# Kernel tuning notes

Hardware: AMD Instinct MI355X
Metric: run time of the kernel (lower is better)

The kernel has to match this reference:

```python
import jax, jax.numpy as jnp
import numpy as np

D_MODEL = 1024
D_CONV = 3

def setup_inputs() -> dict:
    key = jax.random.key(0)
    ks = jax.random.split(key, 16)
    d = D_MODEL
    s = 1.0 / np.sqrt(d)
    inp = {
        'x': jax.random.normal(ks[0], (4, 4096, d), dtype=jnp.float32),
        'Wq_w': jax.random.normal(ks[1], (d, d), dtype=jnp.float32) * s,
        'Wq_b': jnp.zeros((d,), dtype=jnp.float32),
        'Wo_w': jax.random.normal(ks[2], (d, d), dtype=jnp.float32) * s,
        'Wo_b': jnp.zeros((d,), dtype=jnp.float32),
        'Wg_w': jax.random.normal(ks[3], (d, d), dtype=jnp.float32) * s,
        'Wg_b': jnp.zeros((d,), dtype=jnp.float32),
        'wa_w': jax.random.normal(ks[4], (d, d), dtype=jnp.float32) * s,
        'wb_w': jax.random.normal(ks[5], (d, d), dtype=jnp.float32) * s,
        'Wout_w': jax.random.normal(ks[6], (d, d), dtype=jnp.float32) * s,
        'Wout_b': jnp.zeros((d,), dtype=jnp.float32),
        'conv_w': jax.random.normal(ks[7], (d, d, D_CONV), dtype=jnp.float32) * (1.0 / np.sqrt(d * D_CONV)),
        'conv_b': jnp.zeros((d,), dtype=jnp.float32),
    }
    return inp

def _lin(x, w, b=None):
    y = jnp.einsum('bsd,ed->bse', x, w)
    return y if b is None else y + b

def _summ(x_to, x_from, w, scale):
    # gelu -> linear -> softmax over seq -> weighted sum over seq -> broadcast
    a = jax.nn.softmax(_lin(jax.nn.gelu(x_from, approximate=False), w) * scale, axis=-2)
    return jnp.sum(x_to * a, axis=-2, keepdims=True)  # [B,1,d], broadcasts

def reference(x, Wq_w, Wq_b, Wo_w, Wo_b, Wg_w, Wg_b, wa_w, wb_w, Wout_w, Wout_b, conv_w, conv_b):
    d = x.shape[-1]
    scale = 1.0 / jnp.sqrt(jnp.asarray(d, x.dtype))
    Q = _lin(x, Wq_w, Wq_b)
    O = _lin(x, Wo_w, Wo_b)
    G = _lin(x, Wg_w, Wg_b)
    # conv1d over sequence: [B,S,d] -> [B,d,S] -> conv -> back
    qt = jnp.transpose(Q, (0, 2, 1))
    ct = jax.lax.conv_general_dilated(qt, conv_w, window_strides=(1,),
                                      padding=[(D_CONV // 2, D_CONV // 2)],
                                      dimension_numbers=('NCH', 'OIH', 'NCH'))
    ct = ct + conv_b[None, :, None]
    cq = jax.nn.silu(jnp.transpose(ct, (0, 2, 1)))
    P = O * _summ(Q, cq, wa_w, scale)
    L = jax.nn.silu(G) * _summ(P, P, wb_w, scale)
    return _lin(L, Wout_w, Wout_b)
```

## Files before the change

### kernel.cpp

```cpp
#include <hip/hip_runtime.h>
#include <stdint.h>

#define DEV __device__ __forceinline__

typedef unsigned short u16;
typedef unsigned int u32;
typedef unsigned char u8;

typedef __bf16 bf16x8 __attribute__((ext_vector_type(8)));
typedef float f32x4 __attribute__((ext_vector_type(4)));
typedef u16 u16x8 __attribute__((ext_vector_type(8)));
typedef u16 u16x4 __attribute__((ext_vector_type(4)));
typedef u8 u8x8 __attribute__((ext_vector_type(8)));
typedef int i32x4 __attribute__((ext_vector_type(4)));
typedef int i32x8 __attribute__((ext_vector_type(8)));

static_assert(sizeof(bf16x8) == 16, "bf16x8 must be 16B");

#define NT 16384
#define SPAD 4098

DEV u16 f2bf(float f) {
  u32 u = __float_as_uint(f);
  u32 r = u + 0x7FFFu + ((u >> 16) & 1u);
  return (u16)(r >> 16);
}
DEV float bf2f(u16 h) { return __uint_as_float(((u32)h) << 16); }
DEV float siluf(float x) { return x / (1.f + __expf(-x)); }
DEV float geluf(float x) { return 0.5f * x * (1.f + erff(x * 0.70710678118654752f)); }

DEV u8 f2fp8(float f) {
  u32 u = __float_as_uint(f);
  u32 s = (u >> 24) & 0x80u;
  u32 a = u & 0x7FFFFFFFu;
  if (a >= 0x43E00000u) return (u8)(s | 0x7E);
  if (a < 0x3C800000u) {
    float q = __uint_as_float(a) * 512.f;
    u32 m = (u32)(q + 0.5f);
    return (u8)(s | m);
  }
  u32 r = a + 0xFFFFFu + ((a >> 20) & 1u);
  if (r >= 0x43E00000u) return (u8)(s | 0x7E);
  u32 e = (r >> 23) - 120u;
  u32 m = (r >> 20) & 7u;
  return (u8)(s | (e << 3) | m);
}

DEV void gload_lds16(const void* g, void* l) {
  __builtin_amdgcn_global_load_lds((const __attribute__((address_space(1))) void*)g,
                                   (__attribute__((address_space(3))) void*)l,
                                   16, 0, 0);
}

DEV f32x4 mfma_mx(i32x8 a, i32x8 b, f32x4 c) {
  return __builtin_amdgcn_mfma_scale_f32_16x16x128_f8f6f4(
      a, b, c, 0, 0, 0, 0x7F7F7F7Fu, 0, 0x7F7F7F7Fu);
}

__global__ void cvtk(const float* __restrict__ in, u16* __restrict__ out, int n4, float scale) {
  int i = blockIdx.x * 256 + threadIdx.x;
  if (i >= n4) return;
  const float4 v = *(const float4*)(in + (size_t)i * 4);
  u16x4 o;
  o[0] = f2bf(v.x * scale); o[1] = f2bf(v.y * scale);
  o[2] = f2bf(v.z * scale); o[3] = f2bf(v.w * scale);
  *(u16x4*)(out + (size_t)i * 4) = o;
}

__global__ void cvtw4(const float* __restrict__ w0, const float* __restrict__ w1,
                      const float* __restrict__ w2, const float* __restrict__ w3,
                      u16* __restrict__ dst) {
  int idx = blockIdx.x * 256 + threadIdx.x;
  int mat = idx >> 18, within = idx & 262143;
  const float* src = (mat == 0) ? w0 : (mat == 1) ? w1 : (mat == 2) ? w2 : w3;
  const float4 v = *(const float4*)(src + (size_t)within * 4);
  u16x4 o;
  o[0] = f2bf(v.x); o[1] = f2bf(v.y); o[2] = f2bf(v.z); o[3] = f2bf(v.w);
  *(u16x4*)(dst + (size_t)idx * 4) = o;
}

__global__ void cvtw_f8(const float* __restrict__ wa, const float* __restrict__ wb,
                        u8* __restrict__ dst) {
  int idx = blockIdx.x * 256 + threadIdx.x;
  const float* src = (idx >> 18) ? wb : wa;
  int within = idx & 262143;
  const float4 v = *(const float4*)(src + (size_t)within * 4);
  u32 o = (u32)f2fp8(v.x) | ((u32)f2fp8(v.y) << 8) |
          ((u32)f2fp8(v.z) << 16) | ((u32)f2fp8(v.w) << 24);
  *(u32*)(dst + (size_t)idx * 4) = o;
}

__global__ void cvt_convw8(const float* __restrict__ cw, u8* __restrict__ Wc) {
  int i = blockIdx.x * 256 + threadIdx.x;
  int o = i >> 10, d = i & 1023;
  const float* src = cw + ((size_t)o * 1024 + d) * 3;
  u8* dst = Wc + (size_t)o * 3072 + d;
  dst[0]    = f2fp8(src[0]);
  dst[1024] = f2fp8(src[1]);
  dst[2048] = f2fp8(src[2]);
}

__global__ void zero_halo(u16* __restrict__ Qpad) {
  int i = blockIdx.x * 256 + threadIdx.x;
  int r = i >> 10, c = i & 1023;
  int b = r >> 1, side = r & 1;
  size_t row = (size_t)b * SPAD + (side ? (SPAD - 1) : 0);
  Qpad[row * 1024 + c] = 0;
}

__global__ void cvt_q8(const u16* __restrict__ Qpad, u8* __restrict__ Qpad8) {
  size_t idx = (size_t)blockIdx.x * 256 + threadIdx.x;
  size_t base = idx * 8;
  u16x8 v = *(const u16x8*)(Qpad + base);
  u8x8 o;
#pragma unroll
  for (int j = 0; j < 8; ++j) o[j] = f2fp8(bf2f(v[j]));
  *(u8x8*)(Qpad8 + base) = o;
}

template<int MODE>
__global__ __launch_bounds__(256, 2)
void gemm128(const u16* __restrict__ A, const u16* __restrict__ B,
             void* __restrict__ C, const float* __restrict__ bias,
             void* __restrict__ C2, void* __restrict__ C3,
             const float* __restrict__ bias2, const float* __restrict__ bias3,
             int M, int N, int K, int lda)
{
  __shared__ alignas(16) char smem[32768];
  char* sA = smem;
  char* sB = smem + 16384;

  int nwg = gridDim.x;
  int bx = blockIdx.x;
  if ((nwg & 7) == 0) bx = (bx & 7) * (nwg >> 3) + (bx >> 3);
  int GN = N >> 7;
  int bm = bx / GN, bn = bx - bm * GN;
  int m0 = bm << 7, n0 = bn << 7;

  int tid = threadIdx.x;
  int lane = tid & 63, wid = tid >> 6;
  int wm = wid >> 1, wn = wid & 1;

  f32x4 acc[4][4] = {};

  int strow = tid >> 3;
  int stcolb = (tid & 7) << 4;
  size_t ldab = (size_t)lda * 2;
  size_t ldbb = (size_t)K * 2;

  const int KT = K >> 6;
  for (int kt = 0; kt < KT; ++kt) {
    int k0 = kt << 6;
    const char* Ab = (const char*)(A + ((size_t)m0 * (size_t)lda + k0));
    const char* Bb = (const char*)(B + ((size_t)n0 * (size_t)K + k0));
#pragma unroll
    for (int j = 0; j < 4; ++j) {
      int row = j * 32 + strow;
      int sw = (row & 7) << 4;
      gload_lds16(Ab + (size_t)row * ldab + (size_t)(stcolb ^ sw), sA + j * 4096 + wid * 1024);
      gload_lds16(Bb + (size_t)row * ldbb + (size_t)(stcolb ^ sw), sB + j * 4096 + wid * 1024);
    }
    __syncthreads();
#pragma unroll
    for (int kk = 0; kk < 2; ++kk) {
      bf16x8 av[4], bv[4];
      int cb = ((lane >> 4) << 4) + (kk << 6);
#pragma unroll
      for (int i = 0; i < 4; ++i) {
        int r = (wm << 6) + (i << 4) + (lane & 15);
        av[i] = *(const bf16x8*)(sA + r * 128 + (cb ^ ((r & 7) << 4)));
      }
#pragma unroll
      for (int j = 0; j < 4; ++j) {
        int r = (wn << 6) + (j << 4) + (lane & 15);
        bv[j] = *(const bf16x8*)(sB + r * 128 + (cb ^ ((r & 7) << 4)));
      }
#pragma unroll
      for (int i = 0; i < 4; ++i)
#pragma unroll
        for (int j = 0; j < 4; ++j)
          acc[i][j] = __builtin_amdgcn_mfma_f32_16x16x32_bf16(av[i], bv[j], acc[i][j], 0, 0, 0);
    }
    __syncthreads();
  }

#pragma unroll
  for (int i = 0; i < 4; ++i) {
    int rb = m0 + (wm << 6) + (i << 4) + ((lane >> 4) << 2);
#pragma unroll
    for (int j = 0; j < 4; ++j) {
      int n = n0 + (wn << 6) + (j << 4) + (lane & 15);
      if (MODE == 4) {
        int seg = n >> 10, nn = n & 1023;
        const float* bsel = (seg == 0) ? bias : ((seg == 1) ? bias2 : bias3);
        float bs = bsel ? bsel[nn] : 0.f;
#pragma unroll
        for (int r = 0; r < 4; ++r) {
          int t = rb + r;
          u16 h = f2bf(acc[i][j][r] + bs);
          if (seg == 0) {
            size_t row = (size_t)t + 2 * (t >> 12) + 1;
            ((u16*)C)[row * 1024 + nn] = h;
          } else if (seg == 1) {
            ((u16*)C2)[(size_t)t * 1024 + nn] = h;
          } else {
            ((u16*)C3)[(size_t)t * 1024 + nn] = h;
          }
        }
      } else {
        float bs = bias ? bias[n] : 0.f;
#pragma unroll
        for (int r = 0; r < 4; ++r) {
          int t = rb + r;
          float v = acc[i][j][r] + bs;
          ((float*)C)[(size_t)t * N + n] = v;
        }
      }
    }
  }
}

template<int MODE, int VREMAP>
__global__ __launch_bounds__(256, 2)
void gemm128f8(const u8* __restrict__ A, const u8* __restrict__ B,
               void* __restrict__ C, const float* __restrict__ bias, float episcale,
               const u16* __restrict__ vals, float* __restrict__ PZp, float* __restrict__ PNp,
               int M, int N, int K, int lda )
{
  __shared__ alignas(16) char smem[32768];
  char* sA = smem;
  char* sB = smem + 16384;

  int nwg = gridDim.x;
  int bx = blockIdx.x;
  if ((nwg & 7) == 0) bx = (bx & 7) * (nwg >> 3) + (bx >> 3);
  int GN = N >> 7;
  int bm = bx / GN, bn = bx - bm * GN;
  int m0 = bm << 7, n0 = bn << 7;

  int tid = threadIdx.x;
  int lane = tid & 63, wid = tid >> 6;
  int wm = wid >> 1, wn = wid & 1;

  f32x4 acc[4][4] = {};

  int strow = tid >> 3;
  int stcolb = (tid & 7) << 4;
  int bofm = m0 >> 12;

  const int KT = K >> 7;
  for (int kt = 0; kt < KT; ++kt) {
    int k0 = kt << 7;
    const char* Ab;
    if (MODE == 2) {
      int tap = k0 >> 10;
      Ab = (const char*)A + (size_t)(m0 + 2 * bofm + tap) * lda + (k0 & 1023);
    } else {
      Ab = (const char*)A + (size_t)m0 * lda + k0;
    }
    const char* Bb = (const char*)B + (size_t)n0 * K + k0;
#pragma unroll
    for (int j = 0; j < 4; ++j) {
      int row = j * 32 + strow;
      int sw = (row & 7) << 4;
      gload_lds16(Ab + (size_t)row * lda + (size_t)(stcolb ^ sw), sA + j * 4096 + wid * 1024);
      gload_lds16(Bb + (size_t)row * K + (size_t)(stcolb ^ sw), sB + j * 4096 + wid * 1024);
    }
    __syncthreads();
    {
      i32x8 av[4], bv[4];
      int cb = (lane >> 4) << 5;
#pragma unroll
      for (int i = 0; i < 4; ++i) {
        int r = (wm << 6) + (i << 4) + (lane & 15);
        int sw = (r & 7) << 4;
        i32x4 lo = *(const i32x4*)(sA + r * 128 + (cb ^ sw));
        i32x4 hi = *(const i32x4*)(sA + r * 128 + ((cb + 16) ^ sw));
        av[i] = i32x8{lo[0], lo[1], lo[2], lo[3], hi[0], hi[1], hi[2], hi[3]};
      }
#pragma unroll
      for (int j = 0; j < 4; ++j) {
        int r = (wn << 6) + (j << 4) + (lane & 15);
        int sw = (r & 7) << 4;
        i32x4 lo = *(const i32x4*)(sB + r * 128 + (cb ^ sw));
        i32x4 hi = *(const i32x4*)(sB + r * 128 + ((cb + 16) ^ sw));
        bv[j] = i32x8{lo[0], lo[1], lo[2], lo[3], hi[0], hi[1], hi[2], hi[3]};
      }
#pragma unroll
      for (int i = 0; i < 4; ++i)
#pragma unroll
        for (int j = 0; j < 4; ++j)
          acc[i][j] = mfma_mx(av[i], bv[j], acc[i][j]);
    }
    __syncthreads();
  }

  if (MODE == 2) {
#pragma unroll
    for (int i = 0; i < 4; ++i) {
      int rb = m0 + (wm << 6) + (i << 4) + ((lane >> 4) << 2);
#pragma unroll
      for (int j = 0; j < 4; ++j) {
        int n = n0 + (wn << 6) + (j << 4) + (lane & 15);
        float bs = bias ? bias[n] : 0.f;
#pragma unroll
        for (int r = 0; r < 4; ++r) {
          int t = rb + r;
          float v = acc[i][j][r] + bs;
          ((u8*)C)[(size_t)t * N + n] = f2fp8(geluf(siluf(v)));
        }
      }
    }
  } else {
    float zj[4] = {0.f, 0.f, 0.f, 0.f}, nj[4] = {0.f, 0.f, 0.f, 0.f};
#pragma unroll
    for (int i = 0; i < 4; ++i) {
      int rb = m0 + (wm << 6) + (i << 4) + ((lane >> 4) << 2);
#pragma unroll
      for (int j = 0; j < 4; ++j) {
        int n = n0 + (wn << 6) + (j << 4) + (lane & 15);
#pragma unroll
        for (int r = 0; r < 4; ++r) {
          int t = rb + r;
          float w = __expf(acc[i][j][r] * episcale);
          size_t vrow = VREMAP ? ((size_t)t + 2 * (t >> 12) + 1) : (size_t)t;
          float v = bf2f(vals[vrow * 1024 + n]);
          zj[j] += w;
          nj[j] += v * w;
        }
      }
    }
    __syncthreads();
    float2* arr = (float2*)smem;
    int g = (wm << 2) + (lane >> 4);
#pragma unroll
    for (int j = 0; j < 4; ++j) {
      int cl = (wn << 6) + (j << 4) + (lane & 15);
      arr[cl * 8 + g] = make_float2(zj[j], nj[j]);
    }
    __syncthreads();
    if (tid < 128) {
      float Z = 0.f, Nn = 0.f;
#pragma unroll
      for (int g2 = 0; g2 < 8; ++g2) { float2 p = arr[tid * 8 + g2]; Z += p.x; Nn += p.y; }
      size_t o = (size_t)(m0 >> 7) * 1024 + n0 + tid;
      PZp[o] = Z;
      PNp[o] = Nn;
    }
  }
}

__global__ void summ_combine(const float* __restrict__ pz, const float* __restrict__ pn,
                             const float* __restrict__ mul, float* __restrict__ summ)
{
  int idx = blockIdx.x * 256 + threadIdx.x;
  int b = idx >> 10, e = idx & 1023;
  float Z = 0.f, Nn = 0.f;
  for (int bm = b * 32; bm < b * 32 + 32; ++bm) {
    Z += pz[(size_t)bm * 1024 + e];
    Nn += pn[(size_t)bm * 1024 + e];
  }
  float r = Nn / Z;
  summ[idx] = mul ? r * mul[idx] : r;
}

__global__ void pk(const u16* __restrict__ O, const float* __restrict__ s1,
                   u8* __restrict__ GP8)
{
  size_t idx = (size_t)blockIdx.x * 256 + threadIdx.x;
  size_t base = idx * 8;
  int t = (int)(base >> 10);
  int b = t >> 12;
  int e = (int)(base & 1023);
  const float* sp = s1 + b * 1024 + e;
  u16x8 ov = *(const u16x8*)(O + base);
  u8x8 gv;
#pragma unroll
  for (int j = 0; j < 8; ++j) {
    gv[j] = f2fp8(geluf(bf2f(ov[j]) * sp[j]));
  }
  *(u8x8*)(GP8 + base) = gv;
}

__global__ void lk(const u16* __restrict__ G, const float* __restrict__ s2,
                   u16* __restrict__ L)
{
  size_t idx = (size_t)blockIdx.x * 256 + threadIdx.x;
  size_t base = idx * 8;
  int t = (int)(base >> 10);
  int b = t >> 12;
  int e = (int)(base & 1023);
  const float* sp = s2 + b * 1024 + e;
  u16x8 gvv = *(const u16x8*)(G + base);
  u16x8 lv;
#pragma unroll
  for (int j = 0; j < 8; ++j) {
    lv[j] = f2bf(siluf(bf2f(gvv[j])) * sp[j]);
  }
  *(u16x8*)(L + base) = lv;
}

extern "C" void kernel_launch(void* const* d_in, const int* in_sizes, int n_in,
                              void* d_out, int out_size, void* d_ws, size_t ws_size,
                              hipStream_t stream)
{
  const float* x     = (const float*)d_in[0];
  const float* Wq    = (const float*)d_in[1];
  const float* Wqb   = (const float*)d_in[2];
  const float* Wo    = (const float*)d_in[3];
  const float* Wob   = (const float*)d_in[4];
  const float* Wg    = (const float*)d_in[5];
  const float* Wgb   = (const float*)d_in[6];
  const float* wa    = (const float*)d_in[7];
  const float* wb    = (const float*)d_in[8];
  const float* Wout  = (const float*)d_in[9];
  const float* Woutb = (const float*)d_in[10];
  const float* convw = (const float*)d_in[11];
  const float* convb = (const float*)d_in[12];

  char* ws = (char*)d_ws;
  size_t off = 0;
  auto alloc = [&](size_t bytes) -> char* {
    char* p = ws + off;
    off += (bytes + 255) & ~(size_t)255;
    return p;
  };

  u16* QPAD  = (u16*)alloc((size_t)4 * SPAD * 1024 * 2);
  u8*  QPAD8 = (u8*)alloc((size_t)4 * SPAD * 1024);
  u16* OB   = (u16*)alloc((size_t)NT * 1024 * 2);
  u16* GB   = (u16*)alloc((size_t)NT * 1024 * 2);
  u16* XB   = (u16*)alloc((size_t)NT * 1024 * 2);
  u16* WALL = (u16*)alloc((size_t)4 * 1024 * 1024 * 2);
  u8*  WAB8 = (u8*)alloc((size_t)2 * 1024 * 1024);
  u8*  WC8  = (u8*)alloc((size_t)1024 * 3072);
  float* PZb = (float*)alloc((size_t)128 * 1024 * 4);
  float* PNb = (float*)alloc((size_t)128 * 1024 * 4);
  float* S1 = (float*)alloc((size_t)4096 * 4);
  float* S2 = (float*)alloc((size_t)4096 * 4);

  if (off > ws_size) return;

  u16* WQOG   = WALL;
  u16* WOUTB_ = WALL + (size_t)3 * 1048576;
  u8*  WA8    = WAB8;
  u8*  WB8    = WAB8 + (size_t)1048576;

  u8* GA8 = (u8*)XB;
  u8* GP8 = (u8*)XB;
  u16* LB = OB;

  const float scale = 0.03125f;

  cvtk<<<16384, 256, 0, stream>>>(x, XB, 4194304, 1.0f);
  cvtw4<<<4096, 256, 0, stream>>>(Wq, Wo, Wg, Wout, WALL);
  cvtw_f8<<<2048, 256, 0, stream>>>(wa, wb, WAB8);
  cvt_convw8<<<4096, 256, 0, stream>>>(convw, WC8);
  zero_halo<<<32, 256, 0, stream>>>(QPAD);

  gemm128<4><<<128 * 24, 256, 0, stream>>>(XB, WQOG, QPAD, Wqb, OB, GB, Wob, Wgb,
                                           NT, 3072, 1024, 1024);

  cvt_q8<<<8196, 256, 0, stream>>>(QPAD, QPAD8);

  gemm128f8<2, 0><<<128 * 8, 256, 0, stream>>>(QPAD8, WC8, GA8, convb, 1.0f,
                                               nullptr, nullptr, nullptr,
                                               NT, 1024, 3072, 1024);

  gemm128f8<5, 1><<<128 * 8, 256, 0, stream>>>(GA8, WA8, nullptr, nullptr, scale,
                                               QPAD, PZb, PNb,
                                               NT, 1024, 1024, 1024);
  summ_combine<<<16, 256, 0, stream>>>(PZb, PNb, nullptr, S1);

  pk<<<8192, 256, 0, stream>>>(OB, S1, GP8);

  gemm128f8<5, 0><<<128 * 8, 256, 0, stream>>>(GP8, WB8, nullptr, nullptr, scale,
                                               OB, PZb, PNb,
                                               NT, 1024, 1024, 1024);
  summ_combine<<<16, 256, 0, stream>>>(PZb, PNb, S1, S2);

  lk<<<8192, 256, 0, stream>>>(GB, S2, LB);

  gemm128<3><<<128 * 8, 256, 0, stream>>>(LB, WOUTB_, d_out, Woutb, nullptr, nullptr,
                                          nullptr, nullptr, NT, 1024, 1024, 1024);
}
```

Measured before the change: 419.7 us.

## Merge weight-conversion kernels into one launch and change FP8 GEMM LDS swizzle

```diff
diff --git a/kernel.cpp b/kernel.cpp
--- a/kernel.cpp
+++ b/kernel.cpp
@@ -67,45 +67,45 @@
   *(u16x4*)(out + (size_t)i * 4) = o;
 }
 
-__global__ void cvtw4(const float* __restrict__ w0, const float* __restrict__ w1,
-                      const float* __restrict__ w2, const float* __restrict__ w3,
-                      u16* __restrict__ dst) {
-  int idx = blockIdx.x * 256 + threadIdx.x;
-  int mat = idx >> 18, within = idx & 262143;
-  const float* src = (mat == 0) ? w0 : (mat == 1) ? w1 : (mat == 2) ? w2 : w3;
-  const float4 v = *(const float4*)(src + (size_t)within * 4);
-  u16x4 o;
-  o[0] = f2bf(v.x); o[1] = f2bf(v.y); o[2] = f2bf(v.z); o[3] = f2bf(v.w);
-  *(u16x4*)(dst + (size_t)idx * 4) = o;
-}
-
-__global__ void cvtw_f8(const float* __restrict__ wa, const float* __restrict__ wb,
-                        u8* __restrict__ dst) {
-  int idx = blockIdx.x * 256 + threadIdx.x;
-  const float* src = (idx >> 18) ? wb : wa;
-  int within = idx & 262143;
-  const float4 v = *(const float4*)(src + (size_t)within * 4);
-  u32 o = (u32)f2fp8(v.x) | ((u32)f2fp8(v.y) << 8) |
-          ((u32)f2fp8(v.z) << 16) | ((u32)f2fp8(v.w) << 24);
-  *(u32*)(dst + (size_t)idx * 4) = o;
-}
-
-__global__ void cvt_convw8(const float* __restrict__ cw, u8* __restrict__ Wc) {
-  int i = blockIdx.x * 256 + threadIdx.x;
-  int o = i >> 10, d = i & 1023;
-  const float* src = cw + ((size_t)o * 1024 + d) * 3;
-  u8* dst = Wc + (size_t)o * 3072 + d;
-  dst[0]    = f2fp8(src[0]);
-  dst[1024] = f2fp8(src[1]);
-  dst[2048] = f2fp8(src[2]);
-}
-
-__global__ void zero_halo(u16* __restrict__ Qpad) {
-  int i = blockIdx.x * 256 + threadIdx.x;
-  int r = i >> 10, c = i & 1023;
-  int b = r >> 1, side = r & 1;
-  size_t row = (size_t)b * SPAD + (side ? (SPAD - 1) : 0);
-  Qpad[row * 1024 + c] = 0;
+__global__ void cvt_misc(const float* __restrict__ Wq, const float* __restrict__ Wo,
+                         const float* __restrict__ Wg, const float* __restrict__ Wout,
+                         const float* __restrict__ wa, const float* __restrict__ wb,
+                         const float* __restrict__ cw,
+                         u16* __restrict__ WALL, u8* __restrict__ WAB8,
+                         u8* __restrict__ WC8, u16* __restrict__ QPAD)
+{
+  int bid = blockIdx.x, tid = threadIdx.x;
+  if (bid < 4096) {
+    int idx = bid * 256 + tid;
+    int mat = idx >> 18, within = idx & 262143;
+    const float* src = (mat == 0) ? Wq : (mat == 1) ? Wo : (mat == 2) ? Wg : Wout;
+    const float4 v = *(const float4*)(src + (size_t)within * 4);
+    u16x4 o;
+    o[0] = f2bf(v.x); o[1] = f2bf(v.y); o[2] = f2bf(v.z); o[3] = f2bf(v.w);
+    *(u16x4*)(WALL + (size_t)idx * 4) = o;
+  } else if (bid < 6144) {
+    int idx = (bid - 4096) * 256 + tid;
+    const float* src = (idx >> 18) ? wb : wa;
+    int within = idx & 262143;
+    const float4 v = *(const float4*)(src + (size_t)within * 4);
+    u32 o = (u32)f2fp8(v.x) | ((u32)f2fp8(v.y) << 8) |
+            ((u32)f2fp8(v.z) << 16) | ((u32)f2fp8(v.w) << 24);
+    *(u32*)(WAB8 + (size_t)idx * 4) = o;
+  } else if (bid < 10240) {
+    int i = (bid - 6144) * 256 + tid;
+    int o = i >> 10, d = i & 1023;
+    const float* src = cw + ((size_t)o * 1024 + d) * 3;
+    u8* dst = WC8 + (size_t)o * 3072 + d;
+    dst[0]    = f2fp8(src[0]);
+    dst[1024] = f2fp8(src[1]);
+    dst[2048] = f2fp8(src[2]);
+  } else {
+    int i = (bid - 10240) * 256 + tid;
+    int r = i >> 10, c = i & 1023;
+    int b = r >> 1, side = r & 1;
+    size_t row = (size_t)b * SPAD + (side ? (SPAD - 1) : 0);
+    QPAD[row * 1024 + c] = 0;
+  }
 }
 
 __global__ void cvt_q8(const u16* __restrict__ Qpad, u8* __restrict__ Qpad8) {
@@ -262,7 +262,7 @@
 #pragma unroll
     for (int j = 0; j < 4; ++j) {
       int row = j * 32 + strow;
-      int sw = (row & 7) << 4;
+      int sw = (row & 3) << 5;
       gload_lds16(Ab + (size_t)row * lda + (size_t)(stcolb ^ sw), sA + j * 4096 + wid * 1024);
       gload_lds16(Bb + (size_t)row * K + (size_t)(stcolb ^ sw), sB + j * 4096 + wid * 1024);
     }
@@ -273,17 +273,17 @@
 #pragma unroll
       for (int i = 0; i < 4; ++i) {
         int r = (wm << 6) + (i << 4) + (lane & 15);
-        int sw = (r & 7) << 4;
-        i32x4 lo = *(const i32x4*)(sA + r * 128 + (cb ^ sw));
-        i32x4 hi = *(const i32x4*)(sA + r * 128 + ((cb + 16) ^ sw));
+        const char* p = sA + r * 128 + (cb ^ ((r & 3) << 5));
+        i32x4 lo = *(const i32x4*)p;
+        i32x4 hi = *(const i32x4*)(p + 16);
         av[i] = i32x8{lo[0], lo[1], lo[2], lo[3], hi[0], hi[1], hi[2], hi[3]};
       }
 #pragma unroll
       for (int j = 0; j < 4; ++j) {
         int r = (wn << 6) + (j << 4) + (lane & 15);
-        int sw = (r & 7) << 4;
-        i32x4 lo = *(const i32x4*)(sB + r * 128 + (cb ^ sw));
-        i32x4 hi = *(const i32x4*)(sB + r * 128 + ((cb + 16) ^ sw));
+        const char* p = sB + r * 128 + (cb ^ ((r & 3) << 5));
+        i32x4 lo = *(const i32x4*)p;
+        i32x4 hi = *(const i32x4*)(p + 16);
         bv[j] = i32x8{lo[0], lo[1], lo[2], lo[3], hi[0], hi[1], hi[2], hi[3]};
       }
 #pragma unroll
@@ -453,10 +453,8 @@
   const float scale = 0.03125f;
 
   cvtk<<<16384, 256, 0, stream>>>(x, XB, 4194304, 1.0f);
-  cvtw4<<<4096, 256, 0, stream>>>(Wq, Wo, Wg, Wout, WALL);
-  cvtw_f8<<<2048, 256, 0, stream>>>(wa, wb, WAB8);
-  cvt_convw8<<<4096, 256, 0, stream>>>(convw, WC8);
-  zero_halo<<<32, 256, 0, stream>>>(QPAD);
+  cvt_misc<<<10272, 256, 0, stream>>>(Wq, Wo, Wg, Wout, wa, wb, convw,
+                                      WALL, WAB8, WC8, QPAD);
 
   gemm128<4><<<128 * 24, 256, 0, stream>>>(XB, WQOG, QPAD, Wqb, OB, GB, Wob, Wgb,
                                            NT, 3072, 1024, 1024);
```

Result: no change. 412.4 us (-1.7%).
